# Optimization experiments

Measured on AMD Instinct MI355X. Metric: run time of the kernel, lower is better.

## Reference

```python
import jax, jax.numpy as jnp
import numpy as np

N = 100_000      # nodes
E = 1_600_000    # edges (avg degree 16)
D = 32           # feature width (arch = [32, 32, 32])


def setup_inputs() -> dict:
    key = jax.random.key(0)
    ks = jax.random.split(key, 12)
    x = jax.random.normal(ks[0], (N, D), dtype=jnp.float32)
    edge_index = jax.random.randint(ks[1], (2, E), 0, N, dtype=jnp.int32)
    s = 0.1  # weight scale
    inp = {
        "x": x,
        "edge_index": edge_index,
        "W1a": jax.random.normal(ks[2], (D, D), jnp.float32) * s,
        "b1a": jnp.zeros((D,), jnp.float32),
        "W2a": jax.random.normal(ks[3], (D, D), jnp.float32) * s,
        "b2a": jnp.zeros((D,), jnp.float32),
        "W1b": jax.random.normal(ks[4], (D, D), jnp.float32) * s,
        "b1b": jnp.zeros((D,), jnp.float32),
        "W2b": jax.random.normal(ks[5], (D, D), jnp.float32) * s,
        "b2b": jnp.zeros((D,), jnp.float32),
        "op1": 123,
        "op2": 456,
    }
    return inp


def _gcn_layer(x, W, b, src, dst, dis):
    """PyG GCNConv: out = D^{-1/2}(A+I)D^{-1/2} (x W) + b."""
    h = x @ W  # [N, D]
    norm = dis[src] * dis[dst]  # [E]
    agg = jax.ops.segment_sum(h[src] * norm[:, None], dst, num_segments=x.shape[0])
    # self-loop contribution: norm_ii = dis[i]^2
    agg = agg + h * (dis * dis)[:, None]
    return agg + b


def reference(x, edge_index, W1a, b1a, W2a, b2a, W1b, b1b, W2b, b2b, op1, op2):
    src, dst = edge_index[0], edge_index[1]
    # degree at target node, including self-loop (+1)
    deg = jax.ops.segment_sum(jnp.ones((src.shape[0],), x.dtype), dst, num_segments=N) + 1.0
    dis = jax.lax.rsqrt(deg)  # deg^{-1/2}

    def stack(W1, b1, W2, b2):
        h = jax.nn.relu(_gcn_layer(x, W1, b1, src, dst, dis))
        return _gcn_layer(h, W2, b2, src, dst, dis)

    y1 = stack(W1a, b1a, W2a, b2a)  # [N, D]
    y2 = stack(W1b, b1b, W2b, b2b)  # [N, D]
    l1 = jnp.sum(y1[op1] * y1[op2])
    l2 = jnp.sum(y2[op1] * y2[op2])
    return jnp.stack([l1, l2])
```

## Files before the change

### kernel.cpp

```cpp
#include <hip/hip_runtime.h>
#include <hip/hip_bf16.h>

#define DD 32
#define S1CAP 256
#define PERCAP 128
#define E2CAP 1024
#define L2CHUNK 128

__device__ __forceinline__ void s1_insert(int u, int* nidx, int* s1_list,
                                          int* cnt, unsigned char* need) {
    need[u] = 1;
    int old = atomicCAS(&nidx[u], 0, -1);
    if (old == 0) {
        int pos = atomicAdd(&cnt[0], 1);
        if (pos < S1CAP) { s1_list[pos] = u; nidx[u] = pos + 1; }
    }
}

__global__ void k_scan1(const int* __restrict__ ei, int E,
                        const int* __restrict__ op1p, const int* __restrict__ op2p,
                        int* __restrict__ nidx, int* __restrict__ s1_list,
                        int* __restrict__ e2_src, int* __restrict__ e2_w,
                        int* __restrict__ cnt, unsigned char* __restrict__ need) {
    int tid = blockIdx.x * blockDim.x + threadIdx.x;
    int o1 = op1p[0], o2 = op2p[0];
    if (tid == 0) {
        s1_insert(o1, nidx, s1_list, cnt, need);
        s1_insert(o2, nidx, s1_list, cnt, need);
    }
    int base = tid * 4;
    if (base >= E) return;
    if ((E & 3) == 0) {
        int4 d4 = *reinterpret_cast<const int4*>(ei + (size_t)E + base);
        int dv[4] = {d4.x, d4.y, d4.z, d4.w};
#pragma unroll
        for (int k = 0; k < 4; ++k) {
            int d = dv[k];
            if (d == o1 || d == o2) {
                int s = ei[base + k];
                s1_insert(s, nidx, s1_list, cnt, need);
                int p = atomicAdd(&cnt[2], 1);
                if (p < E2CAP) { e2_src[p] = s; e2_w[p] = (d == o2); }
            }
        }
    } else {
        int end = base + 4; if (end > E) end = E;
        for (int e = base; e < end; ++e) {
            int d = ei[(size_t)E + e];
            if (d == o1 || d == o2) {
                int s = ei[e];
                s1_insert(s, nidx, s1_list, cnt, need);
                int p = atomicAdd(&cnt[2], 1);
                if (p < E2CAP) { e2_src[p] = s; e2_w[p] = (d == o2); }
            }
        }
    }
}

__global__ void k_scan2(const int* __restrict__ ei, int E,
                        const int* __restrict__ nidx,
                        int* __restrict__ e1cnt, int* __restrict__ e1buf,
                        unsigned char* __restrict__ need) {
    int tid = blockIdx.x * blockDim.x + threadIdx.x;
    int base = tid * 4;
    if (base >= E) return;
    if ((E & 3) == 0) {
        int4 d4 = *reinterpret_cast<const int4*>(ei + (size_t)E + base);
        int dv[4] = {d4.x, d4.y, d4.z, d4.w};
#pragma unroll
        for (int k = 0; k < 4; ++k) {
            int ix = nidx[dv[k]];
            if (ix > 0) {
                int s = ei[base + k];
                int slot = atomicAdd(&e1cnt[ix - 1], 1);
                if (slot < PERCAP) e1buf[(size_t)(ix - 1) * PERCAP + slot] = s;
                need[s] = 1;
            }
        }
    } else {
        int end = base + 4; if (end > E) end = E;
        for (int e = base; e < end; ++e) {
            int ix = nidx[ei[(size_t)E + e]];
            if (ix > 0) {
                int s = ei[e];
                int slot = atomicAdd(&e1cnt[ix - 1], 1);
                if (slot < PERCAP) e1buf[(size_t)(ix - 1) * PERCAP + slot] = s;
                need[s] = 1;
            }
        }
    }
}

__global__ void k_scan3(const int* __restrict__ ei, int E,
                        const unsigned char* __restrict__ need,
                        int* __restrict__ deg) {
    int tid = blockIdx.x * blockDim.x + threadIdx.x;
    int base = tid * 4;
    if (base >= E) return;
    if ((E & 3) == 0) {
        int4 d4 = *reinterpret_cast<const int4*>(ei + (size_t)E + base);
        int dv[4] = {d4.x, d4.y, d4.z, d4.w};
#pragma unroll
        for (int k = 0; k < 4; ++k) { int d = dv[k]; if (need[d]) atomicAdd(&deg[d], 1); }
    } else {
        int end = base + 4; if (end > E) end = E;
        for (int e = base; e < end; ++e) { int d = ei[(size_t)E + e]; if (need[d]) atomicAdd(&deg[d], 1); }
    }
}

__global__ __launch_bounds__(64)
void k_layer1(const float* __restrict__ x, const int* __restrict__ deg,
              const float* __restrict__ W1a, const float* __restrict__ b1a,
              const float* __restrict__ W1b, const float* __restrict__ b1b,
              const int* __restrict__ s1_list, const int* __restrict__ cnt,
              const int* __restrict__ e1cnt, const int* __restrict__ e1buf,
              float* __restrict__ hA, float* __restrict__ hB) {
    __shared__ float Wsh[2][DD][DD];
    __shared__ int   sidx[PERCAP];
    __shared__ float snrm[PERCAP];
    __shared__ float aggsh[DD];
    int s1n = cnt[0] < S1CAP ? cnt[0] : S1CAP;
    int i = blockIdx.x;
    if (i >= s1n) return;
    int t = threadIdx.x, st = t >> 5, dd = t & 31;
    {
        float* w0 = &Wsh[0][0][0];
        float* w1 = &Wsh[1][0][0];
        for (int j = t; j < DD * DD; j += 64) { w0[j] = W1a[j]; w1[j] = W1b[j]; }
    }
    int u = s1_list[i];
    float dis_u = rsqrtf((float)deg[u] + 1.0f);
    int ci = e1cnt[i]; if (ci > PERCAP) ci = PERCAP;
    for (int j = t; j < ci; j += 64) {
        int s = e1buf[(size_t)i * PERCAP + j];
        sidx[j] = s;
        snrm[j] = rsqrtf((float)deg[s] + 1.0f) * dis_u;
    }
    __syncthreads();
    float agg = dis_u * dis_u * x[(size_t)u * DD + dd];
#pragma unroll 4
    for (int j = 0; j < ci; ++j)
        agg += snrm[j] * x[(size_t)sidx[j] * DD + dd];
    if (t < DD) aggsh[dd] = agg;
    __syncthreads();
    float y = st ? b1b[dd] : b1a[dd];
#pragma unroll
    for (int k = 0; k < DD; ++k) y += aggsh[k] * Wsh[st][k][dd];
    y = fmaxf(y, 0.f);
    (st ? hB : hA)[(size_t)i * DD + dd] = y;
}

__global__ __launch_bounds__(128)
void k_layer2(const int* __restrict__ deg,
              const float* __restrict__ W2a, const float* __restrict__ b2a,
              const float* __restrict__ W2b, const float* __restrict__ b2b,
              const int* __restrict__ op1p, const int* __restrict__ op2p,
              const int* __restrict__ nidx, const int* __restrict__ cnt,
              const int* __restrict__ e2_src, const int* __restrict__ e2_w,
              const float* __restrict__ hA, const float* __restrict__ hB,
              float* __restrict__ out) {
    __shared__ float Wsh[2][DD][DD];
    __shared__ int   prow[L2CHUNK];
    __shared__ int   pw[L2CHUNK];
    __shared__ float pnrm[L2CHUNK];
    __shared__ float aggsh[2][2][DD];
    __shared__ float ysh[2][2][DD];
    int t = threadIdx.x;
    int st = t >> 6, w = (t >> 5) & 1, dd = t & 31;
    {
        float* w0 = &Wsh[0][0][0];
        float* w1 = &Wsh[1][0][0];
        for (int j = t; j < DD * DD; j += 128) { w0[j] = W2a[j]; w1[j] = W2b[j]; }
    }
    int o1 = op1p[0], o2 = op2p[0];
    int v = w ? o2 : o1;
    float dis_v = rsqrtf((float)deg[v] + 1.0f);
    const float* h = st ? hB : hA;
    int rv = nidx[v] - 1; if (rv < 0) rv = 0;
    float agg = dis_v * dis_v * h[(size_t)rv * DD + dd];
    int c2 = cnt[2] < E2CAP ? cnt[2] : E2CAP;
    for (int j0 = 0; j0 < c2; j0 += L2CHUNK) {
        int jn = c2 - j0; if (jn > L2CHUNK) jn = L2CHUNK;
        __syncthreads();
        if (t < jn) {
            int s = e2_src[j0 + t];
            prow[t] = nidx[s] - 1;
            pw[t]   = e2_w[j0 + t];
            pnrm[t] = rsqrtf((float)deg[s] + 1.0f);
        }
        __syncthreads();
#pragma unroll 4
        for (int j = 0; j < jn; ++j) {
            if (pw[j] == w && prow[j] >= 0)
                agg += (pnrm[j] * dis_v) * h[(size_t)prow[j] * DD + dd];
        }
    }
    aggsh[w][st][dd] = agg;
    __syncthreads();
    float y = st ? b2b[dd] : b2a[dd];
#pragma unroll
    for (int k = 0; k < DD; ++k) y += aggsh[w][st][k] * Wsh[st][k][dd];
    ysh[st][w][dd] = y;
    __syncthreads();
    if (t < 2) {
        float sum = 0.f;
        for (int k = 0; k < DD; ++k) sum += ysh[t][0][k] * ysh[t][1][k];
        out[t] = sum;
    }
}

extern "C" void kernel_launch(void* const* d_in, const int* in_sizes, int n_in,
                              void* d_out, int out_size, void* d_ws, size_t ws_size,
                              hipStream_t stream) {
    const float* x   = (const float*)d_in[0];
    const int*   ei  = (const int*)d_in[1];
    const float* W1a = (const float*)d_in[2];
    const float* b1a = (const float*)d_in[3];
    const float* W2a = (const float*)d_in[4];
    const float* b2a = (const float*)d_in[5];
    const float* W1b = (const float*)d_in[6];
    const float* b1b = (const float*)d_in[7];
    const float* W2b = (const float*)d_in[8];
    const float* b2b = (const float*)d_in[9];
    const int* op1 = (const int*)d_in[10];
    const int* op2 = (const int*)d_in[11];
    int N = in_sizes[0] / DD;
    int E = in_sizes[1] / 2;

    char* p = (char*)d_ws;
    int* cnt   = (int*)p;            p += 64;
    int* e1cnt = (int*)p;            p += S1CAP * 4;
    int* deg   = (int*)p;            p += (size_t)N * 4;
    int* nidx  = (int*)p;            p += (size_t)N * 4;
    unsigned char* need = (unsigned char*)p;
    size_t needpad = ((size_t)N + 15) & ~(size_t)15;
    p += needpad;
    size_t zbytes = 64 + S1CAP * 4 + (size_t)N * 8 + needpad;
    int* s1_list = (int*)p;          p += S1CAP * 4;
    int* e1buf   = (int*)p;          p += (size_t)S1CAP * PERCAP * 4;
    int* e2_src  = (int*)p;          p += E2CAP * 4;
    int* e2_w    = (int*)p;          p += E2CAP * 4;
    float* hA    = (float*)p;        p += (size_t)S1CAP * DD * 4;
    float* hB    = (float*)p;        p += (size_t)S1CAP * DD * 4;

    hipMemsetAsync(d_ws, 0, zbytes, stream);

    int nb4 = (int)(((size_t)E / 4 + 256) / 256);
    k_scan1<<<nb4, 256, 0, stream>>>(ei, E, op1, op2, nidx, s1_list, e2_src, e2_w, cnt, need);
    k_scan2<<<nb4, 256, 0, stream>>>(ei, E, nidx, e1cnt, e1buf, need);
    k_scan3<<<nb4, 256, 0, stream>>>(ei, E, need, deg);
    k_layer1<<<S1CAP, 64, 0, stream>>>(x, deg, W1a, b1a, W1b, b1b,
                                       s1_list, cnt, e1cnt, e1buf, hA, hB);
    k_layer2<<<1, 128, 0, stream>>>(deg, W2a, b2a, W2b, b2b, op1, op2,
                                    nidx, cnt, e2_src, e2_w, hA, hB,
                                    (float*)d_out);
}
```

Before: 125.1 us.

## Fuse memset, edge scans and both layers into one cooperative kernel

Replaces the memset plus five separate launches with a single cooperative kernel of 512 blocks. It zeroes the workspace in-kernel and separates the phases with grid-wide syncs, using grid-stride loops over the edge list. The aim is to remove per-launch overhead and inter-kernel gaps, since each phase does little work. The cost is five grid.sync barriers and fewer threads per edge pass. The old multi-kernel path is kept as a fallback and its vectorised branches are simplified to scalar loops.

Result: slower. 429.9 us (+243.6%).

```diff
diff --git a/kernel.cpp b/kernel.cpp
--- a/kernel.cpp
+++ b/kernel.cpp
@@ -1,11 +1,25 @@
 #include <hip/hip_runtime.h>
 #include <hip/hip_bf16.h>
+#include <hip/hip_cooperative_groups.h>
+
+namespace cg = cooperative_groups;
 
 #define DD 32
 #define S1CAP 256
 #define PERCAP 128
 #define E2CAP 1024
-#define L2CHUNK 128
+#define GRID 512
+#define TPB 256
+
+struct Params {
+    const float* x;
+    const int* ei;
+    int E, N;
+    const float *W1a, *b1a, *W2a, *b2a, *W1b, *b1b, *W2b, *b2b;
+    const int *op1p, *op2p;
+    char* ws;
+    float* out;
+};
 
 __device__ __forceinline__ void s1_insert(int u, int* nidx, int* s1_list,
                                           int* cnt, unsigned char* need) {
@@ -14,6 +28,207 @@
     if (old == 0) {
         int pos = atomicAdd(&cnt[0], 1);
         if (pos < S1CAP) { s1_list[pos] = u; nidx[u] = pos + 1; }
+    }
+}
+
+__global__ __launch_bounds__(TPB, 4)
+void k_fused(Params P) {
+    cg::grid_group grid = cg::this_grid();
+    __shared__ float Wsh[2][DD][DD];
+    __shared__ int   sidx[PERCAP];
+    __shared__ float snrm[PERCAP];
+    __shared__ float aggsh[DD];
+    __shared__ int   prow[PERCAP];
+    __shared__ int   pw[PERCAP];
+    __shared__ float pnrm[PERCAP];
+    __shared__ float agg2[2][2][DD];
+    __shared__ float ysh[2][2][DD];
+
+    char* p = P.ws;
+    int* cnt   = (int*)p;            p += 64;
+    int* e1cnt = (int*)p;            p += S1CAP * 4;
+    int* deg   = (int*)p;            p += (size_t)P.N * 4;
+    int* nidx  = (int*)p;            p += (size_t)P.N * 4;
+    unsigned char* need = (unsigned char*)p;
+    size_t needpad = ((size_t)P.N + 15) & ~(size_t)15;
+    p += needpad;
+    int* s1_list = (int*)p;          p += S1CAP * 4;
+    int* e1buf   = (int*)p;          p += (size_t)S1CAP * PERCAP * 4;
+    int* e2_src  = (int*)p;          p += E2CAP * 4;
+    int* e2_w    = (int*)p;          p += E2CAP * 4;
+    float* hA    = (float*)p;        p += (size_t)S1CAP * DD * 4;
+    float* hB    = (float*)p;
+
+    int t = threadIdx.x;
+    int gtid = blockIdx.x * TPB + t;
+    int nth = gridDim.x * TPB;
+    int E = P.E;
+    const int* eis = P.ei;
+    const int* eid = P.ei + (size_t)E;
+    int nchunk = E >> 2;
+    int tail = nchunk << 2;
+
+    {
+        size_t zn16 = (64 + S1CAP * 4 + (size_t)P.N * 8 + needpad) >> 4;
+        int4 z = make_int4(0, 0, 0, 0);
+        int4* zp = (int4*)P.ws;
+        for (size_t j = gtid; j < zn16; j += nth) zp[j] = z;
+    }
+    grid.sync();
+
+    int o1 = P.op1p[0], o2 = P.op2p[0];
+
+    if (gtid == 0) {
+        s1_insert(o1, nidx, s1_list, cnt, need);
+        s1_insert(o2, nidx, s1_list, cnt, need);
+    }
+    for (int c = gtid; c < nchunk; c += nth) {
+        int4 d4 = ((const int4*)eid)[c];
+        int dv[4] = {d4.x, d4.y, d4.z, d4.w};
+#pragma unroll
+        for (int k = 0; k < 4; ++k) {
+            int d = dv[k];
+            if (d == o1 || d == o2) {
+                int s = eis[c * 4 + k];
+                s1_insert(s, nidx, s1_list, cnt, need);
+                int q = atomicAdd(&cnt[2], 1);
+                if (q < E2CAP) { e2_src[q] = s; e2_w[q] = (d == o2); }
+            }
+        }
+    }
+    for (int e = tail + gtid; e < E; e += nth) {
+        int d = eid[e];
+        if (d == o1 || d == o2) {
+            int s = eis[e];
+            s1_insert(s, nidx, s1_list, cnt, need);
+            int q = atomicAdd(&cnt[2], 1);
+            if (q < E2CAP) { e2_src[q] = s; e2_w[q] = (d == o2); }
+        }
+    }
+    grid.sync();
+
+    for (int c = gtid; c < nchunk; c += nth) {
+        int4 d4 = ((const int4*)eid)[c];
+        int dv[4] = {d4.x, d4.y, d4.z, d4.w};
+#pragma unroll
+        for (int k = 0; k < 4; ++k) {
+            int ix = nidx[dv[k]];
+            if (ix > 0) {
+                int s = eis[c * 4 + k];
+                int slot = atomicAdd(&e1cnt[ix - 1], 1);
+                if (slot < PERCAP) e1buf[(size_t)(ix - 1) * PERCAP + slot] = s;
+                need[s] = 1;
+            }
+        }
+    }
+    for (int e = tail + gtid; e < E; e += nth) {
+        int ix = nidx[eid[e]];
+        if (ix > 0) {
+            int s = eis[e];
+            int slot = atomicAdd(&e1cnt[ix - 1], 1);
+            if (slot < PERCAP) e1buf[(size_t)(ix - 1) * PERCAP + slot] = s;
+            need[s] = 1;
+        }
+    }
+    grid.sync();
+
+    for (int c = gtid; c < nchunk; c += nth) {
+        int4 d4 = ((const int4*)eid)[c];
+        int dv[4] = {d4.x, d4.y, d4.z, d4.w};
+#pragma unroll
+        for (int k = 0; k < 4; ++k) { int d = dv[k]; if (need[d]) atomicAdd(&deg[d], 1); }
+    }
+    for (int e = tail + gtid; e < E; e += nth) {
+        int d = eid[e]; if (need[d]) atomicAdd(&deg[d], 1);
+    }
+    grid.sync();
+
+    int s1n = cnt[0] < S1CAP ? cnt[0] : S1CAP;
+
+    if (blockIdx.x < s1n) {
+        int i = blockIdx.x;
+        {
+            float* w0 = &Wsh[0][0][0];
+            float* w1 = &Wsh[1][0][0];
+            for (int j = t; j < DD * DD; j += TPB) { w0[j] = P.W1a[j]; w1[j] = P.W1b[j]; }
+        }
+        int u = s1_list[i];
+        float dis_u = rsqrtf((float)deg[u] + 1.0f);
+        int ci = e1cnt[i]; if (ci > PERCAP) ci = PERCAP;
+        for (int j = t; j < ci; j += TPB) {
+            int s = e1buf[(size_t)i * PERCAP + j];
+            sidx[j] = s;
+            snrm[j] = rsqrtf((float)deg[s] + 1.0f) * dis_u;
+        }
+        __syncthreads();
+        if (t < 64) {
+            int dd = t & 31;
+            float agg = dis_u * dis_u * P.x[(size_t)u * DD + dd];
+#pragma unroll 4
+            for (int j = 0; j < ci; ++j)
+                agg += snrm[j] * P.x[(size_t)sidx[j] * DD + dd];
+            if (t < DD) aggsh[dd] = agg;
+        }
+        __syncthreads();
+        if (t < 64) {
+            int st = t >> 5, dd = t & 31;
+            float y = st ? P.b1b[dd] : P.b1a[dd];
+#pragma unroll
+            for (int k = 0; k < DD; ++k) y += aggsh[k] * Wsh[st][k][dd];
+            y = fmaxf(y, 0.f);
+            (st ? hB : hA)[(size_t)i * DD + dd] = y;
+        }
+    }
+    grid.sync();
+
+    if (blockIdx.x == 0) {
+        {
+            float* w0 = &Wsh[0][0][0];
+            float* w1 = &Wsh[1][0][0];
+            for (int j = t; j < DD * DD; j += TPB) { w0[j] = P.W2a[j]; w1[j] = P.W2b[j]; }
+        }
+        int st = (t >> 6) & 1, w = (t >> 5) & 1, dd = t & 31;
+        int v = w ? o2 : o1;
+        float dis_v = rsqrtf((float)deg[v] + 1.0f);
+        const float* h = st ? hB : hA;
+        float agg = 0.f;
+        if (t < 128) {
+            int rv = nidx[v] - 1; if (rv < 0) rv = 0;
+            agg = dis_v * dis_v * h[(size_t)rv * DD + dd];
+        }
+        int c2 = cnt[2] < E2CAP ? cnt[2] : E2CAP;
+        for (int j0 = 0; j0 < c2; j0 += PERCAP) {
+            int jn = c2 - j0; if (jn > PERCAP) jn = PERCAP;
+            __syncthreads();
+            if (t < jn) {
+                int s = e2_src[j0 + t];
+                prow[t] = nidx[s] - 1;
+                pw[t]   = e2_w[j0 + t];
+                pnrm[t] = rsqrtf((float)deg[s] + 1.0f);
+            }
+            __syncthreads();
+            if (t < 128) {
+#pragma unroll 4
+                for (int j = 0; j < jn; ++j) {
+                    if (pw[j] == w && prow[j] >= 0)
+                        agg += (pnrm[j] * dis_v) * h[(size_t)prow[j] * DD + dd];
+                }
+            }
+        }
+        if (t < 128) agg2[w][st][dd] = agg;
+        __syncthreads();
+        if (t < 128) {
+            float y = st ? P.b2b[dd] : P.b2a[dd];
+#pragma unroll
+            for (int k = 0; k < DD; ++k) y += agg2[w][st][k] * Wsh[st][k][dd];
+            ysh[st][w][dd] = y;
+        }
+        __syncthreads();
+        if (t < 2) {
+            float sum = 0.f;
+            for (int k = 0; k < DD; ++k) sum += ysh[t][0][k] * ysh[t][1][k];
+            P.out[t] = sum;
+        }
     }
 }
 
@@ -30,29 +245,14 @@
     }
     int base = tid * 4;
     if (base >= E) return;
-    if ((E & 3) == 0) {
-        int4 d4 = *reinterpret_cast<const int4*>(ei + (size_t)E + base);
-        int dv[4] = {d4.x, d4.y, d4.z, d4.w};
-#pragma unroll
-        for (int k = 0; k < 4; ++k) {
-            int d = dv[k];
-            if (d == o1 || d == o2) {
-                int s = ei[base + k];
-                s1_insert(s, nidx, s1_list, cnt, need);
-                int p = atomicAdd(&cnt[2], 1);
-                if (p < E2CAP) { e2_src[p] = s; e2_w[p] = (d == o2); }
-            }
-        }
-    } else {
-        int end = base + 4; if (end > E) end = E;
-        for (int e = base; e < end; ++e) {
-            int d = ei[(size_t)E + e];
-            if (d == o1 || d == o2) {
-                int s = ei[e];
-                s1_insert(s, nidx, s1_list, cnt, need);
-                int p = atomicAdd(&cnt[2], 1);
-                if (p < E2CAP) { e2_src[p] = s; e2_w[p] = (d == o2); }
-            }
+    int end = base + 4; if (end > E) end = E;
+    for (int e = base; e < end; ++e) {
+        int d = ei[(size_t)E + e];
+        if (d == o1 || d == o2) {
+            int s = ei[e];
+            s1_insert(s, nidx, s1_list, cnt, need);
+            int p = atomicAdd(&cnt[2], 1);
+            if (p < E2CAP) { e2_src[p] = s; e2_w[p] = (d == o2); }
         }
     }
 }
@@ -64,29 +264,14 @@
     int tid = blockIdx.x * blockDim.x + threadIdx.x;
     int base = tid * 4;
     if (base >= E) return;
-    if ((E & 3) == 0) {
-        int4 d4 = *reinterpret_cast<const int4*>(ei + (size_t)E + base);
-        int dv[4] = {d4.x, d4.y, d4.z, d4.w};
-#pragma unroll
-        for (int k = 0; k < 4; ++k) {
-            int ix = nidx[dv[k]];
-            if (ix > 0) {
-                int s = ei[base + k];
-                int slot = atomicAdd(&e1cnt[ix - 1], 1);
-                if (slot < PERCAP) e1buf[(size_t)(ix - 1) * PERCAP + slot] = s;
-                need[s] = 1;
-            }
-        }
-    } else {
-        int end = base + 4; if (end > E) end = E;
-        for (int e = base; e < end; ++e) {
-            int ix = nidx[ei[(size_t)E + e]];
-            if (ix > 0) {
-                int s = ei[e];
-                int slot = atomicAdd(&e1cnt[ix - 1], 1);
-                if (slot < PERCAP) e1buf[(size_t)(ix - 1) * PERCAP + slot] = s;
-                need[s] = 1;
-            }
+    int end = base + 4; if (end > E) end = E;
+    for (int e = base; e < end; ++e) {
+        int ix = nidx[ei[(size_t)E + e]];
+        if (ix > 0) {
+            int s = ei[e];
+            int slot = atomicAdd(&e1cnt[ix - 1], 1);
+            if (slot < PERCAP) e1buf[(size_t)(ix - 1) * PERCAP + slot] = s;
+            need[s] = 1;
         }
     }
 }
@@ -97,14 +282,9 @@
     int tid = blockIdx.x * blockDim.x + threadIdx.x;
     int base = tid * 4;
     if (base >= E) return;
-    if ((E & 3) == 0) {
-        int4 d4 = *reinterpret_cast<const int4*>(ei + (size_t)E + base);
-        int dv[4] = {d4.x, d4.y, d4.z, d4.w};
-#pragma unroll
-        for (int k = 0; k < 4; ++k) { int d = dv[k]; if (need[d]) atomicAdd(&deg[d], 1); }
-    } else {
-        int end = base + 4; if (end > E) end = E;
-        for (int e = base; e < end; ++e) { int d = ei[(size_t)E + e]; if (need[d]) atomicAdd(&deg[d], 1); }
+    int end = base + 4; if (end > E) end = E;
+    for (int e = base; e < end; ++e) {
+        int d = ei[(size_t)E + e]; if (need[d]) atomicAdd(&deg[d], 1);
     }
 }
 
@@ -160,9 +340,9 @@
               const float* __restrict__ hA, const float* __restrict__ hB,
               float* __restrict__ out) {
     __shared__ float Wsh[2][DD][DD];
-    __shared__ int   prow[L2CHUNK];
-    __shared__ int   pw[L2CHUNK];
-    __shared__ float pnrm[L2CHUNK];
+    __shared__ int   prow[PERCAP];
+    __shared__ int   pw[PERCAP];
+    __shared__ float pnrm[PERCAP];
     __shared__ float aggsh[2][2][DD];
     __shared__ float ysh[2][2][DD];
     int t = threadIdx.x;
@@ -179,8 +359,8 @@
     int rv = nidx[v] - 1; if (rv < 0) rv = 0;
     float agg = dis_v * dis_v * h[(size_t)rv * DD + dd];
     int c2 = cnt[2] < E2CAP ? cnt[2] : E2CAP;
-    for (int j0 = 0; j0 < c2; j0 += L2CHUNK) {
-        int jn = c2 - j0; if (jn > L2CHUNK) jn = L2CHUNK;
+    for (int j0 = 0; j0 < c2; j0 += PERCAP) {
+        int jn = c2 - j0; if (jn > PERCAP) jn = PERCAP;
         __syncthreads();
         if (t < jn) {
             int s = e2_src[j0 + t];
@@ -227,6 +407,19 @@
     int N = in_sizes[0] / DD;
     int E = in_sizes[1] / 2;
 
+    Params P;
+    P.x = x; P.ei = ei; P.E = E; P.N = N;
+    P.W1a = W1a; P.b1a = b1a; P.W2a = W2a; P.b2a = b2a;
+    P.W1b = W1b; P.b1b = b1b; P.W2b = W2b; P.b2b = b2b;
+    P.op1p = op1; P.op2p = op2;
+    P.ws = (char*)d_ws; P.out = (float*)d_out;
+
+    void* args[] = { &P };
+    hipError_t err = hipLaunchCooperativeKernel((const void*)k_fused,
+                                                dim3(GRID), dim3(TPB),
+                                                args, 0, stream);
+    if (err == hipSuccess) return;
+
     char* p = (char*)d_ws;
     int* cnt   = (int*)p;            p += 64;
     int* e1cnt = (int*)p;            p += S1CAP * 4;
@@ -244,7 +437,6 @@
     float* hB    = (float*)p;        p += (size_t)S1CAP * DD * 4;
 
     hipMemsetAsync(d_ws, 0, zbytes, stream);
-
     int nb4 = (int)(((size_t)E / 4 + 256) / 256);
     k_scan1<<<nb4, 256, 0, stream>>>(ei, E, op1, op2, nidx, s1_list, e2_src, e2_w, cnt, need);
     k_scan2<<<nb4, 256, 0, stream>>>(ei, E, nidx, e1cnt, e1buf, need);
```
